# Optimization experiments

Hardware: AMD Instinct MI355X
Metric: run time of the kernel (lower is better)

Reference implementation:

```python
import jax, jax.numpy as jnp
import numpy as np

N_ROWS = 8192
EMBED = 256


def setup_inputs() -> dict:
    key = jax.random.key(0)
    k1, k2, k3, k4, k5 = jax.random.split(key, 5)
    M = jax.random.normal(k1, (N_ROWS, EMBED), dtype=jnp.float32)
    N = jax.random.normal(k2, (N_ROWS, EMBED), dtype=jnp.float32)
    gate_w_weight = jax.random.normal(k3, (1, EMBED), dtype=jnp.float32) * (1.0 / np.sqrt(EMBED))
    gate_w_bias = jax.random.normal(k4, (1,), dtype=jnp.float32)
    gate_b = jax.random.normal(k5, (1,), dtype=jnp.float32)
    return {"M": M, "N": N, "gate_w_weight": gate_w_weight,
            "gate_w_bias": gate_w_bias, "gate_b": gate_b}


def reference(M, N, gate_w_weight, gate_w_bias, gate_b):
    # scores: [n, n] = N @ M^T
    mt = jnp.matmul(N, M.T)
    # zero the diagonal (mt - diag(diag(mt)))
    n = mt.shape[0]
    idx = jnp.arange(n)
    diag_zeroed = mt.at[idx, idx].set(0.0)
    attn = jax.nn.softmax(diag_zeroed, axis=-1)
    out_attn = jnp.matmul(attn, M)  # [n, d]
    # gate: Linear(d -> 1) + extra scalar bias, then sigmoid
    gate_tmp = jnp.matmul(out_attn, gate_w_weight.T) + gate_w_bias + gate_b  # [n, 1]
    gate = jax.nn.sigmoid(gate_tmp)
    boosted = out_attn * gate + N * (1.0 - gate)
    return boosted[:, None, None, :]  # [n, 1, 1, d]
```

## Files before the change

### kernel.cpp

```cpp
#include <hip/hip_runtime.h>
#include <math.h>

#define NR   8192
#define DIM  256
#define QBLK 32

using f32x4  = __attribute__((ext_vector_type(4))) float;
using s4v    = __attribute__((ext_vector_type(4))) short;
using s8v    = __attribute__((ext_vector_type(8))) short;
using bf16x8 = __attribute__((ext_vector_type(8))) short;
typedef _Float16 f16x8 __attribute__((ext_vector_type(8)));
typedef _Float16 f16x4 __attribute__((ext_vector_type(4)));

__device__ __forceinline__ short f2bf(float x){
  union{float f; unsigned u;} v; v.f = x;
  unsigned r = v.u + 0x7fffu + ((v.u >> 16) & 1u);
  return (short)(r >> 16);
}
__device__ __forceinline__ float bf2f(short s){
  union{unsigned u; float f;} v; v.u = ((unsigned)(unsigned short)s) << 16;
  return v.f;
}
__device__ __forceinline__ short f2h(float x){
  union{_Float16 h; short s;} c; c.h = (_Float16)x; return c.s;
}

#define SS_SHORTS 32768
#define WS_BYTES_NEEDED (128u * 32768u * 2u)

#define LDS8_SHORTS 81920

__device__ __forceinline__ void dma16(const short* g, short* l){
  __builtin_amdgcn_global_load_lds(
      (const __attribute__((address_space(1))) unsigned int*)g,
      (__attribute__((address_space(3))) unsigned int*)l, 16, 0, 0);
}

__launch_bounds__(256)
__global__ void precompute_ws(const float* __restrict__ Mp, short* __restrict__ ws)
{
  const int tid = threadIdx.x;
  const int bx  = blockIdx.x;
  const int ss  = bx >> 4;
  const int sub = bx & 15;
  const int fi  = sub*256 + tid;
  const int plane = fi >> 11;
  const int rest  = fi & 2047;
  const int p   = rest >> 10;
  const int cl  = rest & 1023;
  const int ch  = cl >> 6;
  const int l   = cl & 63;
  const int li  = l & 15, g = l >> 4;

  short v[8];
  if (plane == 0){
    const int kk = ch >> 1, n = ch & 1;
    const int row = ss*64 + p*32 + n*16 + li;
    const int d0  = kk*32 + g*8;
    const float* src = Mp + (size_t)row*DIM + d0;
    #pragma unroll
    for (int j = 0; j < 8; ++j) v[j] = f2h(src[j]);
  } else {
    const int u   = p*16 + ch;
    const int par = u >> 3;
    const int np  = u & 7;
    #pragma unroll
    for (int j = 0; j < 8; ++j){
      const int nf = 2*np + (j >> 2);
      const int jj = j & 3;
      const int row = ss*64 + par*16 + (l >> 4)*4 + jj;
      const int col = nf*16 + (l & 15);
      v[j] = f2h(Mp[(size_t)row*DIM + col]);
    }
  }
  s8v ov = {v[0],v[1],v[2],v[3],v[4],v[5],v[6],v[7]};
  *(s8v*)(ws + (size_t)ss*SS_SHORTS + plane*16384 + p*8192 + ch*512 + l*8) = ov;
}

__launch_bounds__(512, 2)
__global__ void attn_gate_v12(const float* __restrict__ Np,
                              const float* __restrict__ gw, const float* __restrict__ gwb,
                              const float* __restrict__ gb,
                              const short* __restrict__ ws, float* __restrict__ out)
{
  extern __shared__ short S_[];
  const int tid  = threadIdx.x;
  const int w    = tid >> 6;
  const int lane = tid & 63;
  const int g    = lane >> 4;
  const int li   = lane & 15;
  const int qsub = w & 1;
  const int par  = w >> 1;
  const int qb   = blockIdx.x * QBLK;
  const int fbase = w * 8;
  const bool isK  = (w < 4);

  f16x8 qh[8];
  {
    const float* qrow = Np + (size_t)(qb + qsub*16 + li) * DIM;
    #pragma unroll
    for (int kk = 0; kk < 8; ++kk){
      const int d0 = kk*32 + g*8;
      #pragma unroll
      for (int j = 0; j < 8; ++j)
        qh[kk][j] = (_Float16)qrow[d0 + j];
    }
  }

  f32x4 o[16];
  #pragma unroll
  for (int nf = 0; nf < 16; ++nf){ f32x4 z = {0.f,0.f,0.f,0.f}; o[nf] = z; }
  float m0 = -1e30f, l0 = 0.0f;

  const int p2 = par >> 1, n2 = par & 1;
  const int kfrag_off = p2*8192 + n2*512 + lane*8;

  int khc = 0;
  int vtr = 65536;
  int vtc = 32768;
  int vtf = 49152;

  {
    const int ldst = isK ? 0 : (32768 - 16384);
    #pragma unroll
    for (int i = 0; i < 8; ++i){
      const int f = fbase + i;
      dma16(ws + (size_t)f*512 + lane*8, S_ + ldst + f*512);
    }
  }
  __syncthreads();

  f16x4 paP;
  paP[0] = (_Float16)0.f; paP[1] = (_Float16)0.f;
  paP[2] = (_Float16)0.f; paP[3] = (_Float16)0.f;

  for (int ss = 0; ss < 128; ++ss){
    const size_t ssb = (size_t)ss * SS_SHORTS;

    if (ss < 127){
      const size_t nsb = ssb + SS_SHORTS;
      const int ldst = isK ? (khc ^ 16384) : (vtf - 16384);
      #pragma unroll
      for (int i = 0; i < 8; ++i){
        const int f = fbase + i;
        dma16(ws + nsb + (size_t)f*512 + lane*8, S_ + ldst + f*512);
      }
    }

    f32x4 sa0, sa1, sa2, sa3;
    { f32x4 z = {0.f,0.f,0.f,0.f}; sa0 = z; sa1 = z; sa2 = z; sa3 = z; }
    {
      const short* kbase = S_ + khc + kfrag_off;
      __builtin_amdgcn_s_setprio(1);
      {
        f16x8 b0 = *(const f16x8*)(kbase);
        f16x8 b1 = *(const f16x8*)(kbase + 1024);
        sa0 = __builtin_amdgcn_mfma_f32_16x16x32_f16(b0, qh[0], sa0, 0, 0, 0);
        sa0 = __builtin_amdgcn_mfma_f32_16x16x32_f16(b1, qh[1], sa0, 0, 0, 0);
      }
      {
        f16x8 b2 = *(const f16x8*)(kbase + 2048);
        f16x8 b3 = *(const f16x8*)(kbase + 3072);
        sa1 = __builtin_amdgcn_mfma_f32_16x16x32_f16(b2, qh[2], sa1, 0, 0, 0);
        sa1 = __builtin_amdgcn_mfma_f32_16x16x32_f16(b3, qh[3], sa1, 0, 0, 0);
      }
      {
        f16x8 b4 = *(const f16x8*)(kbase + 4096);
        f16x8 b5 = *(const f16x8*)(kbase + 5120);
        sa2 = __builtin_amdgcn_mfma_f32_16x16x32_f16(b4, qh[4], sa2, 0, 0, 0);
        sa2 = __builtin_amdgcn_mfma_f32_16x16x32_f16(b5, qh[5], sa2, 0, 0, 0);
      }
      {
        f16x8 b6 = *(const f16x8*)(kbase + 6144);
        f16x8 b7 = *(const f16x8*)(kbase + 7168);
        sa3 = __builtin_amdgcn_mfma_f32_16x16x32_f16(b6, qh[6], sa3, 0, 0, 0);
        sa3 = __builtin_amdgcn_mfma_f32_16x16x32_f16(b7, qh[7], sa3, 0, 0, 0);
      }

      if (ss > 0){
        const short* vbase = S_ + vtr + par*4096 + lane*8;
        #pragma unroll
        for (int np = 0; np < 8; ++np){
          f16x8 v8 = *(const f16x8*)(vbase + np*512);
          f16x4 lo = __builtin_shufflevector(v8, v8, 0, 1, 2, 3);
          f16x4 hi = __builtin_shufflevector(v8, v8, 4, 5, 6, 7);
          o[2*np]   = __builtin_amdgcn_mfma_f32_16x16x16f16(paP, lo, o[2*np],   0, 0, 0);
          o[2*np+1] = __builtin_amdgcn_mfma_f32_16x16x16f16(paP, hi, o[2*np+1], 0, 0, 0);
        }
      }
      __builtin_amdgcn_s_setprio(0);
    }

    const int kvb = ss*64 + par*16 + g*4;
    const int qg  = qb + qsub*16 + li;
    float s_[4];
    #pragma unroll
    for (int i = 0; i < 4; ++i){
      float sv = (sa0[i] + sa1[i]) + (sa2[i] + sa3[i]);
      if (kvb + i == qg) sv = 0.0f;
      s_[i] = sv;
    }
    const float lmax = fmaxf(fmaxf(s_[0], s_[1]), fmaxf(s_[2], s_[3]));
    float sc = 1.0f;
    if (__any((int)(lmax > m0 + 8.0f))){
      float t = lmax;
      t = fmaxf(t, __shfl_xor(t, 16));
      t = fmaxf(t, __shfl_xor(t, 32));
      const float mn = fmaxf(m0, t);
      sc = __expf(m0 - mn);
      m0 = mn;
      float scr[4];
      #pragma unroll
      for (int i = 0; i < 4; ++i) scr[i] = __shfl(sc, g*4 + i);
      #pragma unroll
      for (int nf = 0; nf < 16; ++nf)
        #pragma unroll
        for (int i = 0; i < 4; ++i) o[nf][i] *= scr[i];
    }

    float p_[4];
    #pragma unroll
    for (int i = 0; i < 4; ++i) p_[i] = __expf(s_[i] - m0);
    paP[0] = (_Float16)p_[0]; paP[1] = (_Float16)p_[1];
    paP[2] = (_Float16)p_[2]; paP[3] = (_Float16)p_[3];

    l0 = l0*sc + ((p_[0] + p_[1]) + (p_[2] + p_[3]));

    __syncthreads();

    const int t = vtr; vtr = vtc; vtc = vtf; vtf = t;
    khc ^= 16384;
  }

  {
    const short* vbase = S_ + vtr + par*4096 + lane*8;
    #pragma unroll
    for (int np = 0; np < 8; ++np){
      f16x8 v8 = *(const f16x8*)(vbase + np*512);
      f16x4 lo = __builtin_shufflevector(v8, v8, 0, 1, 2, 3);
      f16x4 hi = __builtin_shufflevector(v8, v8, 4, 5, 6, 7);
      o[2*np]   = __builtin_amdgcn_mfma_f32_16x16x16f16(paP, lo, o[2*np],   0, 0, 0);
      o[2*np+1] = __builtin_amdgcn_mfma_f32_16x16x16f16(paP, hi, o[2*np+1], 0, 0, 0);
    }
  }
  l0 += __shfl_xor(l0, 16);
  l0 += __shfl_xor(l0, 32);
  __syncthreads();

  float mr[4], lr[4];
  #pragma unroll
  for (int i = 0; i < 4; ++i){
    mr[i] = __shfl(m0, g*4 + i);
    lr[i] = __shfl(l0, g*4 + i);
  }

  float* dump = (float*)S_;
  if (par > 0){
    float* dp = dump + (size_t)((par-1)*128 + qsub*64 + lane) * 72;
    #pragma unroll
    for (int i = 0; i < 4; ++i){ dp[i] = mr[i]; dp[4+i] = lr[i]; }
    #pragma unroll
    for (int nf = 0; nf < 16; ++nf)
      #pragma unroll
      for (int i = 0; i < 4; ++i) dp[8 + nf*4 + i] = o[nf][i];
  }
  __syncthreads();
  if (par == 0){
    #pragma unroll
    for (int pp = 0; pp < 3; ++pp){
      const float* dp = dump + (size_t)(pp*128 + qsub*64 + lane) * 72;
      float a[4], b[4];
      #pragma unroll
      for (int i = 0; i < 4; ++i){
        float mb = dp[i], lb = dp[4+i];
        float mm = fmaxf(mr[i], mb);
        a[i] = __expf(mr[i] - mm);
        b[i] = __expf(mb - mm);
        lr[i] = lr[i]*a[i] + lb*b[i];
        mr[i] = mm;
      }
      #pragma unroll
      for (int nf = 0; nf < 16; ++nf)
        #pragma unroll
        for (int i = 0; i < 4; ++i)
          o[nf][i] = o[nf][i]*a[i] + dp[8 + nf*4 + i]*b[i];
    }

    float inv[4];
    #pragma unroll
    for (int i = 0; i < 4; ++i) inv[i] = 1.0f / lr[i];
    #pragma unroll
    for (int nf = 0; nf < 16; ++nf)
      #pragma unroll
      for (int i = 0; i < 4; ++i) o[nf][i] *= inv[i];

    float acc[4] = {0.f, 0.f, 0.f, 0.f};
    #pragma unroll
    for (int nf = 0; nf < 16; ++nf){
      float wv = gw[nf*16 + li];
      #pragma unroll
      for (int i = 0; i < 4; ++i) acc[i] += o[nf][i] * wv;
    }
    const float bias = gwb[0] + gb[0];
    float gt[4];
    #pragma unroll
    for (int i = 0; i < 4; ++i){
      float x = acc[i];
      x += __shfl_xor(x, 1);
      x += __shfl_xor(x, 2);
      x += __shfl_xor(x, 4);
      x += __shfl_xor(x, 8);
      gt[i] = 1.0f / (1.0f + __expf(-(x + bias)));
    }
    #pragma unroll
    for (int i = 0; i < 4; ++i){
      const int grow = qb + qsub*16 + g*4 + i;
      const float* nrow = Np + (size_t)grow * DIM;
      float* orow = out + (size_t)grow * DIM;
      #pragma unroll
      for (int nf = 0; nf < 16; ++nf){
        const int col = nf*16 + li;
        float nv = nrow[col];
        orow[col] = o[nf][i]*gt[i] + nv*(1.0f - gt[i]);
      }
    }
  }
}

#define KH0 0
#define KH1 8448
#define KL0 16896
#define KL1 25344
#define MT0 33792
#define MT1 44032
#define PBO 54272
#define LDS0_SHORTS 56832

__launch_bounds__(256, 1)
__global__ void attn_gate_v0(const float* __restrict__ Mp, const float* __restrict__ Np,
                             const float* __restrict__ gw, const float* __restrict__ gwb,
                             const float* __restrict__ gb, float* __restrict__ out)
{
  extern __shared__ short S_[];
  const int tid  = threadIdx.x;
  const int w    = tid >> 6;
  const int lane = tid & 63;
  const int g    = lane >> 4;
  const int li   = lane & 15;
  const int qsub = w & 1;
  const int par  = w >> 1;
  const int qb   = blockIdx.x * QBLK;

  short* khp = S_ + (par ? KH1 : KH0);
  short* klp = S_ + (par ? KL1 : KL0);
  short* mtp = S_ + (par ? MT1 : MT0);
  short* pb  = S_ + PBO + w * 640;

  bf16x8 qh[8], ql[8];
  {
    const float* qrow = Np + (size_t)(qb + qsub*16 + li) * DIM;
    #pragma unroll
    for (int kk = 0; kk < 8; ++kk){
      const int d0 = kk*32 + g*8;
      #pragma unroll
      for (int j = 0; j < 8; ++j){
        float f = qrow[d0 + j];
        short h = f2bf(f);
        qh[kk][j] = h;
        ql[kk][j] = f2bf(f - bf2f(h));
      }
    }
  }

  f32x4 o[16];
  #pragma unroll
  for (int nf = 0; nf < 16; ++nf){ f32x4 z = {0.f,0.f,0.f,0.f}; o[nf] = z; }
  float m0[4], l0[4];
  #pragma unroll
  for (int i = 0; i < 4; ++i){ m0[i] = -1e30f; l0[i] = 0.0f; }

  const int NSS = NR / 64;
  for (int ss = 0; ss < NSS; ++ss){
    {
      const int r  = tid >> 2;
      const int cb = (tid & 3) << 6;
      const int p  = r >> 5;
      const int rr = r & 31;
      short* kh = S_ + (p ? KH1 : KH0) + rr*264 + cb;
      short* kl = S_ + (p ? KL1 : KL0) + rr*264 + cb;
      short* mt = S_ + (p ? MT1 : MT0) + rr;
      const float* src = Mp + (size_t)(ss*64 + r) * DIM + cb;
      #pragma unroll
      for (int c = 0; c < 64; c += 4){
        const float4 v = *(const float4*)(src + c);
        float fv[4] = {v.x, v.y, v.z, v.w};
        short h[4], lo[4];
        #pragma unroll
        for (int j = 0; j < 4; ++j){
          h[j]  = f2bf(fv[j]);
          lo[j] = f2bf(fv[j] - bf2f(h[j]));
          mt[(cb + c + j) * 40] = h[j];
        }
        s4v hv = {h[0], h[1], h[2], h[3]};
        s4v lv = {lo[0], lo[1], lo[2], lo[3]};
        *(s4v*)(kh + c) = hv;
        *(s4v*)(kl + c) = lv;
      }
    }
    __syncthreads();

    f32x4 sa[2];
    { f32x4 z = {0.f,0.f,0.f,0.f}; sa[0] = z; sa[1] = z; }
    #pragma unroll
    for (int kk = 0; kk < 8; ++kk){
      #pragma unroll
      for (int n = 0; n < 2; ++n){
        const int a = (n*16 + li)*264 + kk*32 + g*8;
        bf16x8 bh = *(const bf16x8*)(khp + a);
        bf16x8 bl = *(const bf16x8*)(klp + a);
        sa[n] = __builtin_amdgcn_mfma_f32_16x16x32_bf16(qh[kk], bh, sa[n], 0, 0, 0);
        sa[n] = __builtin_amdgcn_mfma_f32_16x16x32_bf16(qh[kk], bl, sa[n], 0, 0, 0);
        sa[n] = __builtin_amdgcn_mfma_f32_16x16x32_bf16(ql[kk], bh, sa[n], 0, 0, 0);
      }
    }

    const int kvb   = ss*64 + par*32;
    const int growb = qb + qsub*16 + g*4;
    float s_[2][4];
    #pragma unroll
    for (int n = 0; n < 2; ++n)
      #pragma unroll
      for (int i = 0; i < 4; ++i){
        float sv = sa[n][i];
        if (kvb + n*16 + li == growb + i) sv = 0.0f;
        s_[n][i] = sv;
      }
    float mn[4], sc[4], ps[4];
    bool need = false;
    #pragma unroll
    for (int i = 0; i < 4; ++i){
      float t = fmaxf(s_[0][i], s_[1][i]);
      t = fmaxf(t, __shfl_xor(t, 1));
      t = fmaxf(t, __shfl_xor(t, 2));
      t = fmaxf(t, __shfl_xor(t, 4));
      t = fmaxf(t, __shfl_xor(t, 8));
      mn[i] = fmaxf(m0[i], t);
      sc[i] = __expf(m0[i] - mn[i]);
      need |= (mn[i] != m0[i]);
      m0[i] = mn[i];
    }
    #pragma unroll
    for (int i = 0; i < 4; ++i) ps[i] = 0.0f;
    #pragma unroll
    for (int n = 0; n < 2; ++n)
      #pragma unroll
      for (int i = 0; i < 4; ++i){
        float p = __expf(s_[n][i] - mn[i]);
        ps[i] += p;
        pb[(g*4 + i)*40 + n*16 + li] = f2bf(p);
      }
    #pragma unroll
    for (int i = 0; i < 4; ++i){
      float t = ps[i];
      t += __shfl_xor(t, 1);
      t += __shfl_xor(t, 2);
      t += __shfl_xor(t, 4);
      t += __shfl_xor(t, 8);
      l0[i] = l0[i]*sc[i] + t;
    }
    if (__any((int)need)){
      #pragma unroll
      for (int nf = 0; nf < 16; ++nf)
        #pragma unroll
        for (int i = 0; i < 4; ++i) o[nf][i] *= sc[i];
    }

    bf16x8 pa = *(const bf16x8*)(pb + li*40 + g*8);
    #pragma unroll
    for (int nf = 0; nf < 16; ++nf){
      bf16x8 bv = *(const bf16x8*)(mtp + (nf*16 + li)*40 + g*8);
      o[nf] = __builtin_amdgcn_mfma_f32_16x16x32_bf16(pa, bv, o[nf], 0, 0, 0);
    }
    __syncthreads();
  }

  float* dump = (float*)S_;
  if (par == 1){
    float* dp = dump + (size_t)(qsub*64 + lane) * 72;
    #pragma unroll
    for (int i = 0; i < 4; ++i){ dp[i] = m0[i]; dp[4+i] = l0[i]; }
    #pragma unroll
    for (int nf = 0; nf < 16; ++nf)
      #pragma unroll
      for (int i = 0; i < 4; ++i) dp[8 + nf*4 + i] = o[nf][i];
  }
  __syncthreads();
  if (par == 0){
    const float* dp = dump + (size_t)(qsub*64 + lane) * 72;
    float a[4], b[4];
    #pragma unroll
    for (int i = 0; i < 4; ++i){
      float mb = dp[i], lb = dp[4+i];
      float mm = fmaxf(m0[i], mb);
      a[i] = __expf(m0[i] - mm);
      b[i] = __expf(mb - mm);
      l0[i] = l0[i]*a[i] + lb*b[i];
    }
    #pragma unroll
    for (int nf = 0; nf < 16; ++nf)
      #pragma unroll
      for (int i = 0; i < 4; ++i)
        o[nf][i] = o[nf][i]*a[i] + dp[8 + nf*4 + i]*b[i];

    float inv[4];
    #pragma unroll
    for (int i = 0; i < 4; ++i) inv[i] = 1.0f / l0[i];
    #pragma unroll
    for (int nf = 0; nf < 16; ++nf)
      #pragma unroll
      for (int i = 0; i < 4; ++i) o[nf][i] *= inv[i];

    float t[4] = {0.f, 0.f, 0.f, 0.f};
    #pragma unroll
    for (int nf = 0; nf < 16; ++nf){
      float wv = gw[nf*16 + li];
      #pragma unroll
      for (int i = 0; i < 4; ++i) t[i] += o[nf][i] * wv;
    }
    const float bias = gwb[0] + gb[0];
    float gt[4];
    #pragma unroll
    for (int i = 0; i < 4; ++i){
      float x = t[i];
      x += __shfl_xor(x, 1);
      x += __shfl_xor(x, 2);
      x += __shfl_xor(x, 4);
      x += __shfl_xor(x, 8);
      gt[i] = 1.0f / (1.0f + __expf(-(x + bias)));
    }
    #pragma unroll
    for (int i = 0; i < 4; ++i){
      const int grow = qb + qsub*16 + g*4 + i;
      const float* nrow = Np + (size_t)grow * DIM;
      float* orow = out + (size_t)grow * DIM;
      #pragma unroll
      for (int nf = 0; nf < 16; ++nf){
        const int col = nf*16 + li;
        float nv = nrow[col];
        orow[col] = o[nf][i]*gt[i] + nv*(1.0f - gt[i]);
      }
    }
  }
}

extern "C" void kernel_launch(void* const* d_in, const int* in_sizes, int n_in,
                              void* d_out, int out_size, void* d_ws, size_t ws_size,
                              hipStream_t stream)
{
  const float* Mp  = (const float*)d_in[0];
  const float* Np  = (const float*)d_in[1];
  const float* gw  = (const float*)d_in[2];
  const float* gwb = (const float*)d_in[3];
  const float* gb  = (const float*)d_in[4];
  float* out = (float*)d_out;

  if (ws_size >= (size_t)WS_BYTES_NEEDED){
    short* ws = (short*)d_ws;
    precompute_ws<<<128*16, 256, 0, stream>>>(Mp, ws);
    const size_t shmem = (size_t)LDS8_SHORTS * sizeof(short);
    (void)hipFuncSetAttribute((const void*)attn_gate_v12,
                        hipFuncAttributeMaxDynamicSharedMemorySize, (int)shmem);
    attn_gate_v12<<<NR / QBLK, 512, shmem, stream>>>(Np, gw, gwb, gb, ws, out);
  } else {
    const size_t shmem = (size_t)LDS0_SHORTS * sizeof(short);
    (void)hipFuncSetAttribute((const void*)attn_gate_v0,
                        hipFuncAttributeMaxDynamicSharedMemorySize, (int)shmem);
    attn_gate_v0<<<NR / QBLK, 256, shmem, stream>>>(Mp, Np, gw, gwb, gb, out);
  }
}
```

Measured before the change: 163.2 us.

## Load V fragments directly from global into registers instead of staging through LDS

V tiles were previously DMA'd into a triple-buffered LDS ring and read back for the PV MFMAs. Now each wave reads its V fragments straight from the precomputed workspace in global memory into registers at the top of each iteration. Only K is still double-buffered in LDS, so each wave issues half as many DMAs and the LDS footprint shrinks. The cost is direct global-load latency sitting in the loop, relying on L2 hits and on the K MFMAs to hide it, plus extra register pressure from holding eight V vectors.

```diff
diff --git a/kernel.cpp b/kernel.cpp
--- a/kernel.cpp
+++ b/kernel.cpp
@@ -28,7 +28,7 @@
 #define SS_SHORTS 32768
 #define WS_BYTES_NEEDED (128u * 32768u * 2u)
 
-#define LDS8_SHORTS 81920
+#define LDS9_SHORTS 55296
 
 __device__ __forceinline__ void dma16(const short* g, short* l){
   __builtin_amdgcn_global_load_lds(
@@ -78,7 +78,7 @@
 }
 
 __launch_bounds__(512, 2)
-__global__ void attn_gate_v12(const float* __restrict__ Np,
+__global__ void attn_gate_v13(const float* __restrict__ Np,
                               const float* __restrict__ gw, const float* __restrict__ gwb,
                               const float* __restrict__ gb,
                               const short* __restrict__ ws, float* __restrict__ out)
@@ -92,8 +92,7 @@
   const int qsub = w & 1;
   const int par  = w >> 1;
   const int qb   = blockIdx.x * QBLK;
-  const int fbase = w * 8;
-  const bool isK  = (w < 4);
+  const int fbase = w * 4;
 
   f16x8 qh[8];
   {
@@ -114,19 +113,14 @@
 
   const int p2 = par >> 1, n2 = par & 1;
   const int kfrag_off = p2*8192 + n2*512 + lane*8;
+  const size_t voff = 16384 + par*4096 + lane*8;
 
   int khc = 0;
-  int vtr = 65536;
-  int vtc = 32768;
-  int vtf = 49152;
-
-  {
-    const int ldst = isK ? 0 : (32768 - 16384);
-    #pragma unroll
-    for (int i = 0; i < 8; ++i){
-      const int f = fbase + i;
-      dma16(ws + (size_t)f*512 + lane*8, S_ + ldst + f*512);
-    }
+
+  #pragma unroll
+  for (int i = 0; i < 4; ++i){
+    const int f = fbase + i;
+    dma16(ws + (size_t)f*512 + lane*8, S_ + f*512);
   }
   __syncthreads();
 
@@ -137,11 +131,19 @@
   for (int ss = 0; ss < 128; ++ss){
     const size_t ssb = (size_t)ss * SS_SHORTS;
 
+    f16x8 vv[8];
+    if (ss > 0){
+      const short* vws = ws + (ssb - SS_SHORTS) + voff;
+      #pragma unroll
+      for (int np = 0; np < 8; ++np)
+        vv[np] = *(const f16x8*)(vws + np*512);
+    }
+
     if (ss < 127){
       const size_t nsb = ssb + SS_SHORTS;
-      const int ldst = isK ? (khc ^ 16384) : (vtf - 16384);
-      #pragma unroll
-      for (int i = 0; i < 8; ++i){
+      const int ldst = khc ^ 16384;
+      #pragma unroll
+      for (int i = 0; i < 4; ++i){
         const int f = fbase + i;
         dma16(ws + nsb + (size_t)f*512 + lane*8, S_ + ldst + f*512);
       }
@@ -178,12 +180,10 @@
       }
 
       if (ss > 0){
-        const short* vbase = S_ + vtr + par*4096 + lane*8;
         #pragma unroll
         for (int np = 0; np < 8; ++np){
-          f16x8 v8 = *(const f16x8*)(vbase + np*512);
-          f16x4 lo = __builtin_shufflevector(v8, v8, 0, 1, 2, 3);
-          f16x4 hi = __builtin_shufflevector(v8, v8, 4, 5, 6, 7);
+          f16x4 lo = __builtin_shufflevector(vv[np], vv[np], 0, 1, 2, 3);
+          f16x4 hi = __builtin_shufflevector(vv[np], vv[np], 4, 5, 6, 7);
           o[2*np]   = __builtin_amdgcn_mfma_f32_16x16x16f16(paP, lo, o[2*np],   0, 0, 0);
           o[2*np+1] = __builtin_amdgcn_mfma_f32_16x16x16f16(paP, hi, o[2*np+1], 0, 0, 0);
         }
@@ -228,15 +228,14 @@
 
     __syncthreads();
 
-    const int t = vtr; vtr = vtc; vtc = vtf; vtf = t;
     khc ^= 16384;
   }
 
   {
-    const short* vbase = S_ + vtr + par*4096 + lane*8;
+    const short* vws = ws + (size_t)127 * SS_SHORTS + voff;
     #pragma unroll
     for (int np = 0; np < 8; ++np){
-      f16x8 v8 = *(const f16x8*)(vbase + np*512);
+      f16x8 v8 = *(const f16x8*)(vws + np*512);
       f16x4 lo = __builtin_shufflevector(v8, v8, 0, 1, 2, 3);
       f16x4 hi = __builtin_shufflevector(v8, v8, 4, 5, 6, 7);
       o[2*np]   = __builtin_amdgcn_mfma_f32_16x16x16f16(paP, lo, o[2*np],   0, 0, 0);
@@ -567,10 +566,10 @@
   if (ws_size >= (size_t)WS_BYTES_NEEDED){
     short* ws = (short*)d_ws;
     precompute_ws<<<128*16, 256, 0, stream>>>(Mp, ws);
-    const size_t shmem = (size_t)LDS8_SHORTS * sizeof(short);
-    (void)hipFuncSetAttribute((const void*)attn_gate_v12,
+    const size_t shmem = (size_t)LDS9_SHORTS * sizeof(short);
+    (void)hipFuncSetAttribute((const void*)attn_gate_v13,
                         hipFuncAttributeMaxDynamicSharedMemorySize, (int)shmem);
-    attn_gate_v12<<<NR / QBLK, 512, shmem, stream>>>(Np, gw, gwb, gb, ws, out);
+    attn_gate_v13<<<NR / QBLK, 512, shmem, stream>>>(Np, gw, gwb, gb, ws, out);
   } else {
     const size_t shmem = (size_t)LDS0_SHORTS * sizeof(short);
     (void)hipFuncSetAttribute((const void*)attn_gate_v0,
```

After: 197.9 us. 1.21x slower.
